# Kernel tuning notes

Measured on AMD Instinct MI355X. Metric: run time of the kernel, lower is better.

## Reference

```python
import jax, jax.numpy as jnp
import numpy as np

H = 1024          # hidden_size
E = 2             # expand factor
D = H * E         # d_inner = 2048
N = 16            # state_size
K = 4             # conv kernel
R = H // 16       # dt_rank = 64
B_SZ = 2
L = 1024
EPS = 1e-6


def setup_inputs() -> dict:
    key = jax.random.key(0)
    ks = jax.random.split(key, 12)
    s = 0.02
    inputs = jax.random.normal(ks[0], (B_SZ, L, H), jnp.float32)
    current_state = jnp.zeros((B_SZ, D, N), jnp.float32)
    norm_w = jnp.ones((H,), jnp.float32)
    in_proj_w = jax.random.normal(ks[1], (2 * D, H), jnp.float32) * s
    in_proj_b = jnp.zeros((2 * D,), jnp.float32)
    conv_w = jax.random.normal(ks[2], (D, 1, K), jnp.float32) * 0.2
    conv_b = jnp.zeros((D,), jnp.float32)
    x_proj_w = jax.random.normal(ks[3], (R + 2 * N, D), jnp.float32) * s
    x_proj_b = jnp.zeros((R + 2 * N,), jnp.float32)
    dt_proj_w = jax.random.normal(ks[4], (D, R), jnp.float32) * s
    dt_proj_b = jnp.zeros((D,), jnp.float32)
    A_log = jnp.log(jnp.tile(jnp.arange(1, N + 1, dtype=jnp.float32)[None, :], (D, 1)))
    D_param = jnp.ones((D,), jnp.float32)
    out_proj_w = jax.random.normal(ks[5], (H, D), jnp.float32) * s
    out_proj_b = jnp.zeros((H,), jnp.float32)
    return dict(inputs=inputs, current_state=current_state, norm_w=norm_w,
                in_proj_w=in_proj_w, in_proj_b=in_proj_b, conv_w=conv_w, conv_b=conv_b,
                x_proj_w=x_proj_w, x_proj_b=x_proj_b, dt_proj_w=dt_proj_w, dt_proj_b=dt_proj_b,
                A_log=A_log, D_param=D_param, out_proj_w=out_proj_w, out_proj_b=out_proj_b)


def _rmsnorm(x, w, eps=EPS):
    var = jnp.mean(x * x, axis=-1, keepdims=True)
    return x * jax.lax.rsqrt(var + eps) * w


def _ssm_forward(inputs, current_state, norm_w, in_proj_w, in_proj_b, conv_w, conv_b,
                 x_proj_w, x_proj_b, dt_proj_w, dt_proj_b, A_log, D_param,
                 out_proj_w, out_proj_b):
    residual = inputs  # standard residual: connect_width -> (inputs, None)
    x = _rmsnorm(inputs, norm_w)                                   # [B,L,H]
    xg = jnp.einsum('blh,oh->blo', x, in_proj_w) + in_proj_b       # [B,L,2D]
    x, gate = jnp.split(xg, 2, axis=-1)                            # each [B,L,D]
    # depthwise causal conv: torch pads K-1 both sides then slices [:L] == left-pad K-1
    xc = jax.lax.conv_general_dilated(
        x.transpose(0, 2, 1), conv_w, window_strides=(1,),
        padding=[(K - 1, 0)], dimension_numbers=('NCH', 'OIH', 'NCH'),
        feature_group_count=D) + conv_b[None, :, None]
    x = jax.nn.silu(xc.transpose(0, 2, 1))                         # [B,L,D]
    proj = jnp.einsum('bld,od->blo', x, x_proj_w) + x_proj_b       # [B,L,R+2N]
    dt, Bm, Cm = proj[..., :R], proj[..., R:R + N], proj[..., R + N:]
    delta = jax.nn.softplus(jnp.einsum('blr,dr->bld', dt, dt_proj_w) + dt_proj_b)  # [B,L,D]
    A = -jnp.exp(A_log)                                            # [D,N]
    log_deltaA = delta[..., None] * A                              # [B,L,D,N] (== log(exp(.)))
    cumsum_deltaA = jnp.exp(jnp.cumsum(log_deltaA, axis=1))        # [B,L,D,N]
    h0_contribution = current_state[:, None] * cumsum_deltaA
    shifted = jnp.concatenate(
        [jnp.ones_like(cumsum_deltaA[:, :1]), cumsum_deltaA[:, :-1]], axis=1)
    deltaB_x = delta[..., None] * Bm[:, :, None, :] * x[..., None] # [B,L,D,N]
    scaled = deltaB_x / jnp.clip(shifted, 1e-10)
    h = jnp.cumsum(scaled, axis=1) * shifted + h0_contribution     # [B,L,D,N]
    y = jnp.sum(h * Cm[:, :, None, :], axis=-1) + x * D_param      # [B,L,D]
    y = y * jax.nn.silu(gate)
    out = jnp.einsum('bld,hd->blh', y, out_proj_w) + out_proj_b    # [B,L,H]
    return residual + out


def reference(inputs, current_state, norm_w, in_proj_w, in_proj_b, conv_w, conv_b,
              x_proj_w, x_proj_b, dt_proj_w, dt_proj_b, A_log, D_param,
              out_proj_w, out_proj_b):
    return _ssm_forward(inputs, current_state, norm_w, in_proj_w, in_proj_b,
                        conv_w, conv_b, x_proj_w, x_proj_b, dt_proj_w, dt_proj_b,
                        A_log, D_param, out_proj_w, out_proj_b)
```

## Files before the change

kernel.cpp:

```cpp
#include <hip/hip_runtime.h>
#include <stdint.h>

#define LSEQ 1024
#define HDIM 1024
#define DDIM 2048
#define BL 2048
#define NST 16
#define XR 1027

typedef unsigned short u16;
typedef __attribute__((ext_vector_type(8))) short bf16x8;
typedef __attribute__((ext_vector_type(4))) float f32x4;

static __device__ __forceinline__ float silu_f(float v) {
  return v * __builtin_amdgcn_rcpf(1.f + __expf(-v));
}
static __device__ __forceinline__ float bf2f(u16 u) {
  union { float f; unsigned int i; } c; c.i = ((unsigned int)u) << 16; return c.f;
}
static __device__ __forceinline__ u16 f2bf(float f) {
  union { float f; unsigned int i; } c; c.f = f;
  unsigned int r = c.i + 0x7fffu + ((c.i >> 16) & 1u);
  return (u16)(r >> 16);
}
static __device__ __forceinline__ float softplus_f(float v) {
  return (v > 20.f) ? v : __logf(1.f + __expf(v));
}

__global__ __launch_bounds__(256) void k_castw(const float* __restrict__ src,
                                               u16* __restrict__ dst) {
  int idx = blockIdx.x * 256 + threadIdx.x;
  float4 v = ((const float4*)src)[idx];
  ushort4 o;
  o.x = f2bf(v.x); o.y = f2bf(v.y); o.z = f2bf(v.z); o.w = f2bf(v.w);
  ((ushort4*)dst)[idx] = o;
}

__global__ __launch_bounds__(256) void k_castsplit(const float* __restrict__ src,
                                                   u16* __restrict__ hi,
                                                   u16* __restrict__ lo) {
  int idx = blockIdx.x * 256 + threadIdx.x;
  float4 v = ((const float4*)src)[idx];
  ushort4 h, l;
  h.x = f2bf(v.x); l.x = f2bf(v.x - bf2f(h.x));
  h.y = f2bf(v.y); l.y = f2bf(v.y - bf2f(h.y));
  h.z = f2bf(v.z); l.z = f2bf(v.z - bf2f(h.z));
  h.w = f2bf(v.w); l.w = f2bf(v.w - bf2f(h.w));
  ((ushort4*)hi)[idx] = h;
  ((ushort4*)lo)[idx] = l;
}

__global__ __launch_bounds__(256) void k_zerohalo(u16* __restrict__ xgb) {
  int idx = blockIdx.x * 256 + threadIdx.x;
  int b = idx / 3072;
  int r = idx - b * 3072;
  ushort4 z4 = {0, 0, 0, 0};
  ((ushort4*)(xgb + (size_t)b * XR * 4096))[r] = z4;
}

__global__ __launch_bounds__(256) void k_rowscale2(const float* __restrict__ inp,
                                                   const float* __restrict__ nw,
                                                   u16* __restrict__ xnb) {
  int row = blockIdx.x;
  int t = threadIdx.x;
  float4 xv = *(const float4*)(inp + (size_t)row * HDIM + t * 4);
  float ss = xv.x * xv.x + xv.y * xv.y + xv.z * xv.z + xv.w * xv.w;
  for (int off = 32; off > 0; off >>= 1) ss += __shfl_down(ss, off);
  __shared__ float red[4];
  if ((t & 63) == 0) red[t >> 6] = ss;
  __syncthreads();
  float tot = red[0] + red[1] + red[2] + red[3];
  float scale = rsqrtf(tot * (1.f / HDIM) + 1e-6f);
  float4 nv = *(const float4*)(nw + t * 4);
  ushort4 o;
  o.x = f2bf(xv.x * scale * nv.x); o.y = f2bf(xv.y * scale * nv.y);
  o.z = f2bf(xv.z * scale * nv.z); o.w = f2bf(xv.w * scale * nv.w);
  ((ushort4*)xnb)[row * 256 + t] = o;
}

__global__ __launch_bounds__(256) void k_gemm1b(const u16* __restrict__ A,
                                                const u16* __restrict__ W,
                                                const float* __restrict__ bias,
                                                u16* __restrict__ xgb) {
  __shared__ u16 Asm[128 * 40];
  __shared__ u16 Wsm[128 * 40];
  int t = threadIdx.x;
  int m0 = blockIdx.y * 128, n0 = blockIdx.x * 128;
  int srow = t >> 1, koff = (t & 1) * 16;
  const u16* Ag = A + (size_t)(m0 + srow) * HDIM + koff;
  const u16* Wg = W + (size_t)(n0 + srow) * HDIM + koff;
  int w = t >> 6, lane = t & 63;
  int wr = w >> 1, wc = w & 1;
  int quad = lane >> 4, mr = lane & 15;
  f32x4 z = {0.f, 0.f, 0.f, 0.f};
  f32x4 acc[4][4] = {{z, z, z, z}, {z, z, z, z}, {z, z, z, z}, {z, z, z, z}};
  const u16* arp = &Asm[(wr * 64 + mr) * 40 + quad * 8];
  const u16* brp = &Wsm[(wc * 64 + mr) * 40 + quad * 8];
  for (int k0 = 0; k0 < HDIM; k0 += 32) {
    uint4 a0 = *(const uint4*)(Ag + k0);
    uint4 a1 = *(const uint4*)(Ag + k0 + 8);
    uint4 w0 = *(const uint4*)(Wg + k0);
    uint4 w1 = *(const uint4*)(Wg + k0 + 8);
    __syncthreads();
    *(uint4*)(&Asm[srow * 40 + koff]) = a0;
    *(uint4*)(&Asm[srow * 40 + koff + 8]) = a1;
    *(uint4*)(&Wsm[srow * 40 + koff]) = w0;
    *(uint4*)(&Wsm[srow * 40 + koff + 8]) = w1;
    __syncthreads();
    bf16x8 af[4], bf[4];
#pragma unroll
    for (int i = 0; i < 4; i++) {
      af[i] = *(const bf16x8*)(arp + i * 16 * 40);
      bf[i] = *(const bf16x8*)(brp + i * 16 * 40);
    }
#pragma unroll
    for (int mi = 0; mi < 4; mi++)
#pragma unroll
      for (int ni = 0; ni < 4; ni++)
        acc[mi][ni] = __builtin_amdgcn_mfma_f32_16x16x32_bf16(af[mi], bf[ni],
                                                              acc[mi][ni], 0, 0, 0);
  }
#pragma unroll
  for (int ni = 0; ni < 4; ni++) {
    int col = n0 + wc * 64 + ni * 16 + mr;
    float bv = bias[col];
#pragma unroll
    for (int mi = 0; mi < 4; mi++) {
#pragma unroll
      for (int rr2 = 0; rr2 < 4; rr2++) {
        int rr = m0 + wr * 64 + mi * 16 + quad * 4 + rr2;
        int row = (rr >> 10) * XR + 3 + (rr & 1023);
        xgb[(size_t)row * 4096 + col] = f2bf(acc[mi][ni][rr2] + bv);
      }
    }
  }
}

__global__ __launch_bounds__(256) void k_gemm2b(const u16* __restrict__ A,
                                                const u16* __restrict__ W,
                                                const float* __restrict__ bias,
                                                const float* __restrict__ resid,
                                                float* __restrict__ out) {
  __shared__ u16 Asm[128 * 40];
  __shared__ u16 Wsm[64 * 40];
  int t = threadIdx.x;
  int m0 = blockIdx.y * 128, n0 = blockIdx.x * 64;
  int srow = t >> 1, koff = (t & 1) * 16;
  const u16* Ag = A + (size_t)(m0 + srow) * DDIM + koff;
  const u16* Wg = W + (size_t)(n0 + (srow & 63)) * DDIM + koff;
  int w = t >> 6, lane = t & 63;
  int wr = w >> 1, wc = w & 1;
  int quad = lane >> 4, mr = lane & 15;
  f32x4 z = {0.f, 0.f, 0.f, 0.f};
  f32x4 acc[4][2] = {{z, z}, {z, z}, {z, z}, {z, z}};
  const u16* arp = &Asm[(wr * 64 + mr) * 40 + quad * 8];
  const u16* brp = &Wsm[(wc * 32 + mr) * 40 + quad * 8];
  for (int k0 = 0; k0 < DDIM; k0 += 32) {
    uint4 a0 = *(const uint4*)(Ag + k0);
    uint4 a1 = *(const uint4*)(Ag + k0 + 8);
    uint4 w0, w1;
    if (t < 128) {
      w0 = *(const uint4*)(Wg + k0);
      w1 = *(const uint4*)(Wg + k0 + 8);
    }
    __syncthreads();
    *(uint4*)(&Asm[srow * 40 + koff]) = a0;
    *(uint4*)(&Asm[srow * 40 + koff + 8]) = a1;
    if (t < 128) {
      *(uint4*)(&Wsm[srow * 40 + koff]) = w0;
      *(uint4*)(&Wsm[srow * 40 + koff + 8]) = w1;
    }
    __syncthreads();
    bf16x8 af[4], bf[2];
#pragma unroll
    for (int i = 0; i < 4; i++) af[i] = *(const bf16x8*)(arp + i * 16 * 40);
#pragma unroll
    for (int i = 0; i < 2; i++) bf[i] = *(const bf16x8*)(brp + i * 16 * 40);
#pragma unroll
    for (int mi = 0; mi < 4; mi++)
#pragma unroll
      for (int ni = 0; ni < 2; ni++)
        acc[mi][ni] = __builtin_amdgcn_mfma_f32_16x16x32_bf16(af[mi], bf[ni],
                                                              acc[mi][ni], 0, 0, 0);
  }
#pragma unroll
  for (int ni = 0; ni < 2; ni++) {
    int col = n0 + wc * 32 + ni * 16 + mr;
    float bv = bias[col];
#pragma unroll
    for (int mi = 0; mi < 4; mi++) {
#pragma unroll
      for (int rr2 = 0; rr2 < 4; rr2++) {
        int row = m0 + wr * 64 + mi * 16 + quad * 4 + rr2;
        out[(size_t)row * HDIM + col] =
            acc[mi][ni][rr2] + bv + resid[(size_t)row * HDIM + col];
      }
    }
  }
}

__global__ __launch_bounds__(256) void k_xprojT(const u16* __restrict__ xgb,
                                                const u16* __restrict__ whb,
                                                const u16* __restrict__ wlb,
                                                const float* __restrict__ cw,
                                                const float* __restrict__ cb,
                                                float* __restrict__ projT,
                                                float* __restrict__ pscr) {
  __shared__ u16 Xst[67 * 40];
  __shared__ u16 XH[64 * 40];
  __shared__ u16 XL[64 * 40];
  __shared__ u16 WH[96 * 40];
  __shared__ u16 WL[96 * 40];
  int t = threadIdx.x;
  int tt = blockIdx.x & 31, ks = blockIdx.x >> 5;
  int tokbase = tt << 6;
  int b = tokbase >> 10, l0 = tokbase & 1023;
  int kbase = ks << 7;
  const u16* xbase = xgb + (size_t)(b * XR + l0) * 4096;
  float* outp = (ks == 0) ? projT : (pscr + (size_t)(ks - 1) * 196608);
  int dlane = t & 31, tokg = t >> 5;
  int wvq = t >> 6, lane = t & 63;
  int quad = lane >> 4, mr = lane & 15;
  f32x4 z = {0.f, 0.f, 0.f, 0.f};
  f32x4 acc[6] = {z, z, z, z, z, z};

  for (int it = 0; it < 4; it++) {
    int kc = kbase + (it << 5);
    for (int idx = t; idx < 268; idx += 256) {
      int r = idx >> 2, p = idx & 3;
      uint4 v = *(const uint4*)(xbase + (size_t)r * 4096 + kc + p * 8);
      *(uint4*)(&Xst[r * 40 + p * 8]) = v;
    }
    for (int idx = t; idx < 384; idx += 256) {
      int r = idx >> 2, p = idx & 3;
      *(uint4*)(&WH[r * 40 + p * 8]) = *(const uint4*)(whb + (size_t)r * 2048 + kc + p * 8);
      *(uint4*)(&WL[r * 40 + p * 8]) = *(const uint4*)(wlb + (size_t)r * 2048 + kc + p * 8);
    }
    __syncthreads();
    {
      int d = kc + dlane;
      float4 cwv = *(const float4*)(cw + d * 4);
      float cbv = cb[d];
      float xr[11];
#pragma unroll
      for (int j = 0; j < 11; j++) xr[j] = bf2f(Xst[(tokg * 8 + j) * 40 + dlane]);
#pragma unroll
      for (int jj = 0; jj < 8; jj++) {
        float xc = silu_f(cbv + cwv.x * xr[jj] + cwv.y * xr[jj + 1] +
                          cwv.z * xr[jj + 2] + cwv.w * xr[jj + 3]);
        u16 h = f2bf(xc);
        u16 l = f2bf(xc - bf2f(h));
        XH[(tokg * 8 + jj) * 40 + dlane] = h;
        XL[(tokg * 8 + jj) * 40 + dlane] = l;
      }
    }
    __syncthreads();
    bf16x8 xh = *(const bf16x8*)(&XH[(wvq * 16 + mr) * 40 + quad * 8]);
    bf16x8 xl = *(const bf16x8*)(&XL[(wvq * 16 + mr) * 40 + quad * 8]);
#pragma unroll
    for (int mi = 0; mi < 6; mi++) {
      bf16x8 wh = *(const bf16x8*)(&WH[(mi * 16 + mr) * 40 + quad * 8]);
      bf16x8 wl = *(const bf16x8*)(&WL[(mi * 16 + mr) * 40 + quad * 8]);
      acc[mi] = __builtin_amdgcn_mfma_f32_16x16x32_bf16(wh, xh, acc[mi], 0, 0, 0);
      acc[mi] = __builtin_amdgcn_mfma_f32_16x16x32_bf16(wh, xl, acc[mi], 0, 0, 0);
      acc[mi] = __builtin_amdgcn_mfma_f32_16x16x32_bf16(wl, xh, acc[mi], 0, 0, 0);
    }
    __syncthreads();
  }
#pragma unroll
  for (int mi = 0; mi < 6; mi++) {
#pragma unroll
    for (int rr = 0; rr < 4; rr++) {
      int o = mi * 16 + quad * 4 + rr;
      outp[(size_t)o * BL + tokbase + wvq * 16 + mr] = acc[mi][rr];
    }
  }
}

__global__ __launch_bounds__(256) void k_xcomb(float* __restrict__ projT,
                                               const float* __restrict__ scr,
                                               const float* __restrict__ xpb) {
  int idx = blockIdx.x * 256 + threadIdx.x;
  int o = idx >> 9;
  float4 a = ((const float4*)projT)[idx];
  float bv = xpb[o];
  float sx = bv, sy = bv, sz = bv, sw = bv;
#pragma unroll
  for (int p = 0; p < 15; p++) {
    float4 s = ((const float4*)(scr + (size_t)p * 196608))[idx];
    sx += s.x; sy += s.y; sz += s.z; sw += s.w;
  }
  a.x += sx; a.y += sy; a.z += sz; a.w += sw;
  ((float4*)projT)[idx] = a;
}

__global__ __launch_bounds__(256) void k_delta(const float* __restrict__ projT,
                                               const float* __restrict__ dtw,
                                               const float* __restrict__ dtb,
                                               float* __restrict__ deltaT) {
  __shared__ float dw_s[16][64];
  int t = threadIdx.x;
  int d0 = (blockIdx.x >> 3) * 16;
  int tokbase = (blockIdx.x & 7) * 256;
  {
    const float* src = dtw + (size_t)d0 * 64;
#pragma unroll
    for (int i = 0; i < 4; i++) {
      int idx = t + i * 256;
      dw_s[idx >> 6][idx & 63] = src[idx];
    }
  }
  __syncthreads();
  int tq = t & 63, dq = t >> 6;
  const float* pr = projT + tokbase + tq * 4;
  int dbase = d0 + dq * 4;
  float acc[4][4];
#pragma unroll
  for (int di = 0; di < 4; di++) {
    float bv = dtb[dbase + di];
    acc[di][0] = bv; acc[di][1] = bv; acc[di][2] = bv; acc[di][3] = bv;
  }
#pragma unroll 8
  for (int r = 0; r < 64; r++) {
    float4 pv = *(const float4*)(pr + (size_t)r * BL);
#pragma unroll
    for (int di = 0; di < 4; di++) {
      float wk = dw_s[dq * 4 + di][r];
      acc[di][0] += pv.x * wk; acc[di][1] += pv.y * wk;
      acc[di][2] += pv.z * wk; acc[di][3] += pv.w * wk;
    }
  }
#pragma unroll
  for (int di = 0; di < 4; di++) {
    float4 o;
    o.x = softplus_f(acc[di][0]); o.y = softplus_f(acc[di][1]);
    o.z = softplus_f(acc[di][2]); o.w = softplus_f(acc[di][3]);
    *(float4*)(deltaT + (size_t)(dbase + di) * BL + tokbase + tq * 4) = o;
  }
}

__global__ __launch_bounds__(256) void k_scan2(const float* __restrict__ projT,
                                               const float* __restrict__ deltaT,
                                               const u16* __restrict__ xgb,
                                               const float* __restrict__ cw,
                                               const float* __restrict__ cb,
                                               const float* __restrict__ alog,
                                               const float* __restrict__ dparam,
                                               const float* __restrict__ cs,
                                               u16* __restrict__ yb) {
  __shared__ float wtot[4];
  __shared__ float xcp[1088];
  __shared__ float uvl[1088];
  __shared__ float dlp[1088];

  int t = threadIdx.x;
  int cidx = ((blockIdx.x & 7) << 9) | (blockIdx.x >> 3);
  int b = cidx >> 11;
  int d = cidx & (DDIM - 1);
  int wv = t >> 6, lane = t & 63;

  float4 cwv = *(const float4*)(cw + d * 4);
  float cbv = cb[d];
  float Dp = dparam[d];
  const u16* xcol = xgb + (size_t)(b * XR + 3) * 4096 + d;
  const u16* gcol = xcol + DDIM;
  u16* ycol = yb + ((size_t)(b << 10)) * DDIM + d;
  int colbase = b << 10;
  int tok0 = t << 2;

  float4 dv = *(const float4*)(deltaT + (size_t)d * BL + colbase + tok0);

  float* xls = dlp;
  if (t < 3) xls[t] = 0.f;
#pragma unroll
  for (int k = 0; k < 4; k++) {
    int tok = t + (k << 8);
    xls[3 + tok] = bf2f(xcol[(size_t)tok * 4096]);
  }
  __syncthreads();

#pragma unroll
  for (int i = 0; i < 4; i++) {
    int tok = tok0 + i;
    float xc = silu_f(cbv + cwv.x * xls[tok] + cwv.y * xls[tok + 1] +
                      cwv.z * xls[tok + 2] + cwv.w * xls[tok + 3]);
    xcp[((tok >> 4) * 17) + (tok & 15)] = xc;
  }
  float d0 = dv.x, d1 = dv.y, d2 = dv.z, d3 = dv.w;
  uvl[((tok0 >> 4) * 17) + (tok0 & 15)]             = d0;
  uvl[(((tok0 + 1) >> 4) * 17) + ((tok0 + 1) & 15)] = d1;
  uvl[(((tok0 + 2) >> 4) * 17) + ((tok0 + 2) & 15)] = d2;
  uvl[(((tok0 + 3) >> 4) * 17) + ((tok0 + 3) & 15)] = d3;
  float c0 = d0, c1 = c0 + d1, c2 = c1 + d2, c3 = c2 + d3;
  float sc = c3;
#pragma unroll
  for (int off = 1; off < 64; off <<= 1) {
    float u = __shfl_up(sc, off);
    if (lane >= off) sc += u;
  }
  if (lane == 63) wtot[wv] = sc;
  __syncthreads();
  {
    float base = sc - c3;
#pragma unroll
    for (int i = 0; i < 3; i++) if (i < wv) base += wtot[i];
    dlp[((tok0 >> 4) * 17) + (tok0 & 15)]             = base + c0;
    dlp[(((tok0 + 1) >> 4) * 17) + ((tok0 + 1) & 15)] = base + c1;
    dlp[(((tok0 + 2) >> 4) * 17) + ((tok0 + 2) & 15)] = base + c2;
    dlp[(((tok0 + 3) >> 4) * 17) + ((tok0 + 3) & 15)] = base + c3;
  }
#pragma unroll
  for (int i = 0; i < 4; i++) {
    int tok = tok0 + i;
    int p = ((tok >> 4) * 17) + (tok & 15);
    uvl[p] = uvl[p] * xcp[p];
  }
  __syncthreads();

  int pb = lane * 17;
  float y[16];
#pragma unroll
  for (int i = 0; i < 16; i++) y[i] = 0.f;
  float Dprev = (lane == 0) ? 0.f : dlp[pb - 2];

#pragma unroll 1
  for (int r = 0; r < 4; r++) {
    int n = (wv << 2) + r;
    float An = -__expf(alog[d * NST + n]);
    float st = cs[(size_t)(b * DDIM + d) * NST + n];
    const float* pB = projT + (size_t)(64 + n) * BL + colbase + (lane << 4);
    const float* pC = pB + (size_t)16 * BL;
    float Pp = __expf(An * Dprev);
    float sl = 0.f;
#pragma unroll
    for (int c = 0; c < 4; c++) {
      float4 bv = *(const float4*)(pB + c * 4);
      float4 cv = *(const float4*)(pC + c * 4);
      float bvs[4] = {bv.x, bv.y, bv.z, bv.w};
      float cvs[4] = {cv.x, cv.y, cv.z, cv.w};
#pragma unroll
      for (int j = 0; j < 4; j++) {
        int i = c * 4 + j;
        float P = __expf(An * dlp[pb + i]);
        float w = uvl[pb + i] * bvs[j] * __builtin_amdgcn_rcpf(fmaxf(Pp, 1e-10f));
        sl += w;
        y[i] += (sl * Pp + st * P) * cvs[j];
        Pp = P;
      }
    }
    float s2 = sl;
#pragma unroll
    for (int off = 1; off < 64; off <<= 1) {
      float u = __shfl_up(s2, off);
      if (lane >= off) s2 += u;
    }
    float Soff = s2 - sl;
#pragma unroll
    for (int c = 0; c < 4; c++) {
      float4 cv = *(const float4*)(pC + c * 4);
      float cvs[4] = {cv.x, cv.y, cv.z, cv.w};
#pragma unroll
      for (int j = 0; j < 4; j++) {
        int i = c * 4 + j;
        float dlm = (i == 0) ? Dprev : dlp[pb + i - 1];
        y[i] += Soff * __expf(An * dlm) * cvs[j];
      }
    }
  }
  __syncthreads();
  if (wv == 2) {
#pragma unroll
    for (int i = 0; i < 16; i++) uvl[pb + i] = y[i];
  } else if (wv == 3) {
#pragma unroll
    for (int i = 0; i < 16; i++) dlp[pb + i] = y[i];
  }
  __syncthreads();
  if (wv == 0) {
#pragma unroll
    for (int i = 0; i < 16; i++) uvl[pb + i] += y[i];
  } else if (wv == 1) {
#pragma unroll
    for (int i = 0; i < 16; i++) dlp[pb + i] += y[i];
  }
  __syncthreads();
#pragma unroll
  for (int i = 0; i < 4; i++) {
    int tok = tok0 + i;
    int p = ((tok >> 4) * 17) + (tok & 15);
    float yv = uvl[p] + dlp[p] + xcp[p] * Dp;
    float g = bf2f(gcol[(size_t)tok * 4096]);
    ycol[(size_t)tok * DDIM] = f2bf(yv * silu_f(g));
  }
}

extern "C" void kernel_launch(void* const* d_in, const int* in_sizes, int n_in,
                              void* d_out, int out_size, void* d_ws, size_t ws_size,
                              hipStream_t stream) {
  const float* inp    = (const float*)d_in[0];
  const float* cstate = (const float*)d_in[1];
  const float* norm_w = (const float*)d_in[2];
  const float* w1     = (const float*)d_in[3];
  const float* b1     = (const float*)d_in[4];
  const float* convw  = (const float*)d_in[5];
  const float* convb  = (const float*)d_in[6];
  const float* xpw    = (const float*)d_in[7];
  const float* xpb    = (const float*)d_in[8];
  const float* dtw    = (const float*)d_in[9];
  const float* dtb    = (const float*)d_in[10];
  const float* alog   = (const float*)d_in[11];
  const float* dparam = (const float*)d_in[12];
  const float* wo     = (const float*)d_in[13];
  const float* bo     = (const float*)d_in[14];
  float* out = (float*)d_out;

  char* wsb = (char*)d_ws;
  u16*   w1b    = (u16*)(wsb + 0);
  u16*   wob    = (u16*)(wsb + 8388608);
  u16*   whb    = (u16*)(wsb + 12591104);
  u16*   wlb    = (u16*)(wsb + 12984320);
  float* projT  = (float*)(wsb + 13377536);
  u16*   xgb    = (u16*)(wsb + 14163968);
  u16*   yb     = (u16*)(wsb + 30990336);
  u16*   xnb    = yb;
  float* deltaT = (float*)(wsb + 39378944);
  float* pscr   = deltaT;

  k_castw<<<4096, 256, 0, stream>>>(w1, w1b);
  k_castw<<<2048, 256, 0, stream>>>(wo, wob);
  k_castsplit<<<192, 256, 0, stream>>>(xpw, whb, wlb);
  k_rowscale2<<<BL, 256, 0, stream>>>(inp, norm_w, xnb);
  k_gemm1b<<<dim3(32, 16), 256, 0, stream>>>(xnb, w1b, b1, xgb);
  k_zerohalo<<<24, 256, 0, stream>>>(xgb);
  k_xprojT<<<512, 256, 0, stream>>>(xgb, whb, wlb, convw, convb, projT, pscr);
  k_xcomb<<<192, 256, 0, stream>>>(projT, pscr, xpb);
  k_delta<<<1024, 256, 0, stream>>>(projT, dtw, dtb, deltaT);
  k_scan2<<<2 * DDIM, 256, 0, stream>>>(projT, deltaT, xgb, convw, convb,
                                        alog, dparam, cstate, yb);
  k_gemm2b<<<dim3(16, 16), 256, 0, stream>>>(yb, wob, bo, inp, out);
}
```

Baseline: 290.6 us.

## Fuse prep kernels, pre-transpose x for scan, split-K the out projection

Merges the three weight-cast kernels and the halo zeroing into one launch. Adds a tiled transpose kernel so the scan reads the x column contiguously instead of with a 4096-element stride. Splits the output projection GEMM into two K halves so twice as many blocks run, then sums the partials with bias and residual in a separate combine kernel. This trades extra launches and partial-sum traffic for better occupancy and coalescing, and reuses the w1b and deltaT workspace regions once they are no longer needed.

```diff
diff --git a/kernel.cpp b/kernel.cpp
--- a/kernel.cpp
+++ b/kernel.cpp
@@ -27,35 +27,45 @@
   return (v > 20.f) ? v : __logf(1.f + __expf(v));
 }
 
-__global__ __launch_bounds__(256) void k_castw(const float* __restrict__ src,
-                                               u16* __restrict__ dst) {
-  int idx = blockIdx.x * 256 + threadIdx.x;
-  float4 v = ((const float4*)src)[idx];
-  ushort4 o;
-  o.x = f2bf(v.x); o.y = f2bf(v.y); o.z = f2bf(v.z); o.w = f2bf(v.w);
-  ((ushort4*)dst)[idx] = o;
-}
-
-__global__ __launch_bounds__(256) void k_castsplit(const float* __restrict__ src,
-                                                   u16* __restrict__ hi,
-                                                   u16* __restrict__ lo) {
-  int idx = blockIdx.x * 256 + threadIdx.x;
-  float4 v = ((const float4*)src)[idx];
-  ushort4 h, l;
-  h.x = f2bf(v.x); l.x = f2bf(v.x - bf2f(h.x));
-  h.y = f2bf(v.y); l.y = f2bf(v.y - bf2f(h.y));
-  h.z = f2bf(v.z); l.z = f2bf(v.z - bf2f(h.z));
-  h.w = f2bf(v.w); l.w = f2bf(v.w - bf2f(h.w));
-  ((ushort4*)hi)[idx] = h;
-  ((ushort4*)lo)[idx] = l;
-}
-
-__global__ __launch_bounds__(256) void k_zerohalo(u16* __restrict__ xgb) {
-  int idx = blockIdx.x * 256 + threadIdx.x;
-  int b = idx / 3072;
-  int r = idx - b * 3072;
-  ushort4 z4 = {0, 0, 0, 0};
-  ((ushort4*)(xgb + (size_t)b * XR * 4096))[r] = z4;
+__global__ __launch_bounds__(256) void k_prep(const float* __restrict__ w1,
+                                              u16* __restrict__ w1b,
+                                              const float* __restrict__ wo,
+                                              u16* __restrict__ wob,
+                                              const float* __restrict__ xpw,
+                                              u16* __restrict__ whb,
+                                              u16* __restrict__ wlb,
+                                              u16* __restrict__ xgb) {
+  int bidx = blockIdx.x;
+  int t = threadIdx.x;
+  if (bidx < 4096) {
+    int idx = bidx * 256 + t;
+    float4 v = ((const float4*)w1)[idx];
+    ushort4 o;
+    o.x = f2bf(v.x); o.y = f2bf(v.y); o.z = f2bf(v.z); o.w = f2bf(v.w);
+    ((ushort4*)w1b)[idx] = o;
+  } else if (bidx < 6144) {
+    int idx = (bidx - 4096) * 256 + t;
+    float4 v = ((const float4*)wo)[idx];
+    ushort4 o;
+    o.x = f2bf(v.x); o.y = f2bf(v.y); o.z = f2bf(v.z); o.w = f2bf(v.w);
+    ((ushort4*)wob)[idx] = o;
+  } else if (bidx < 6336) {
+    int idx = (bidx - 6144) * 256 + t;
+    float4 v = ((const float4*)xpw)[idx];
+    ushort4 h, l;
+    h.x = f2bf(v.x); l.x = f2bf(v.x - bf2f(h.x));
+    h.y = f2bf(v.y); l.y = f2bf(v.y - bf2f(h.y));
+    h.z = f2bf(v.z); l.z = f2bf(v.z - bf2f(h.z));
+    h.w = f2bf(v.w); l.w = f2bf(v.w - bf2f(h.w));
+    ((ushort4*)whb)[idx] = h;
+    ((ushort4*)wlb)[idx] = l;
+  } else {
+    int idx = (bidx - 6336) * 256 + t;
+    int b = idx / 3072;
+    int r = idx - b * 3072;
+    ushort4 z4 = {0, 0, 0, 0};
+    ((ushort4*)(xgb + (size_t)b * XR * 4096))[r] = z4;
+  }
 }
 
 __global__ __launch_bounds__(256) void k_rowscale2(const float* __restrict__ inp,
@@ -136,18 +146,47 @@
   }
 }
 
+__global__ __launch_bounds__(256) void k_xT(const u16* __restrict__ xgb,
+                                            u16* __restrict__ xT) {
+  __shared__ u16 tile[64][66];
+  int dt = blockIdx.x & 31;
+  int tt = blockIdx.x >> 5;
+  int gtok0 = tt << 6;
+  int b = gtok0 >> 10, l0 = gtok0 & 1023;
+  int d0 = dt << 6;
+  int t = threadIdx.x;
+  const u16* src = xgb + (size_t)(b * XR + 3 + l0) * 4096 + d0;
+#pragma unroll
+  for (int i = 0; i < 8; i++) {
+    int idx = t + i * 256;
+    int row = idx >> 5, uc = idx & 31;
+    unsigned int v = *(const unsigned int*)(src + (size_t)row * 4096 + uc * 2);
+    tile[row][uc * 2]     = (u16)(v & 0xffffu);
+    tile[row][uc * 2 + 1] = (u16)(v >> 16);
+  }
+  __syncthreads();
+#pragma unroll
+  for (int i = 0; i < 8; i++) {
+    int idx = t + i * 256;
+    int r = idx >> 5, c2 = idx & 31;
+    unsigned int lo = tile[c2 * 2][r];
+    unsigned int hi = tile[c2 * 2 + 1][r];
+    *(unsigned int*)(xT + (size_t)(d0 + r) * 2048 + gtok0 + c2 * 2) = lo | (hi << 16);
+  }
+}
+
 __global__ __launch_bounds__(256) void k_gemm2b(const u16* __restrict__ A,
                                                 const u16* __restrict__ W,
-                                                const float* __restrict__ bias,
-                                                const float* __restrict__ resid,
-                                                float* __restrict__ out) {
+                                                float* __restrict__ psplit) {
   __shared__ u16 Asm[128 * 40];
   __shared__ u16 Wsm[64 * 40];
   int t = threadIdx.x;
   int m0 = blockIdx.y * 128, n0 = blockIdx.x * 64;
+  int kstart = blockIdx.z << 10;
+  float* outp = psplit + (size_t)blockIdx.z * 2048 * 1024;
   int srow = t >> 1, koff = (t & 1) * 16;
-  const u16* Ag = A + (size_t)(m0 + srow) * DDIM + koff;
-  const u16* Wg = W + (size_t)(n0 + (srow & 63)) * DDIM + koff;
+  const u16* Ag = A + (size_t)(m0 + srow) * DDIM + kstart + koff;
+  const u16* Wg = W + (size_t)(n0 + (srow & 63)) * DDIM + kstart + koff;
   int w = t >> 6, lane = t & 63;
   int wr = w >> 1, wc = w & 1;
   int quad = lane >> 4, mr = lane & 15;
@@ -155,7 +194,7 @@
   f32x4 acc[4][2] = {{z, z}, {z, z}, {z, z}, {z, z}};
   const u16* arp = &Asm[(wr * 64 + mr) * 40 + quad * 8];
   const u16* brp = &Wsm[(wc * 32 + mr) * 40 + quad * 8];
-  for (int k0 = 0; k0 < DDIM; k0 += 32) {
+  for (int k0 = 0; k0 < 1024; k0 += 32) {
     uint4 a0 = *(const uint4*)(Ag + k0);
     uint4 a1 = *(const uint4*)(Ag + k0 + 8);
     uint4 w0, w1;
@@ -186,17 +225,33 @@
 #pragma unroll
   for (int ni = 0; ni < 2; ni++) {
     int col = n0 + wc * 32 + ni * 16 + mr;
-    float bv = bias[col];
 #pragma unroll
     for (int mi = 0; mi < 4; mi++) {
 #pragma unroll
       for (int rr2 = 0; rr2 < 4; rr2++) {
         int row = m0 + wr * 64 + mi * 16 + quad * 4 + rr2;
-        out[(size_t)row * HDIM + col] =
-            acc[mi][ni][rr2] + bv + resid[(size_t)row * HDIM + col];
+        outp[(size_t)row * 1024 + col] = acc[mi][ni][rr2];
       }
     }
   }
+}
+
+__global__ __launch_bounds__(256) void k_ocomb(const float* __restrict__ psplit,
+                                               const float* __restrict__ bias,
+                                               const float* __restrict__ resid,
+                                               float* __restrict__ out) {
+  int idx = blockIdx.x * 256 + threadIdx.x;
+  int colf = idx & 255;
+  float4 a = ((const float4*)psplit)[idx];
+  float4 b2 = ((const float4*)(psplit + 2048 * 1024))[idx];
+  float4 rv = ((const float4*)resid)[idx];
+  float4 bv = *(const float4*)(bias + colf * 4);
+  float4 o;
+  o.x = a.x + b2.x + bv.x + rv.x;
+  o.y = a.y + b2.y + bv.y + rv.y;
+  o.z = a.z + b2.z + bv.z + rv.z;
+  o.w = a.w + b2.w + bv.w + rv.w;
+  ((float4*)out)[idx] = o;
 }
 
 __global__ __launch_bounds__(256) void k_xprojT(const u16* __restrict__ xgb,
@@ -341,6 +396,7 @@
 
 __global__ __launch_bounds__(256) void k_scan2(const float* __restrict__ projT,
                                                const float* __restrict__ deltaT,
+                                               const u16* __restrict__ xT,
                                                const u16* __restrict__ xgb,
                                                const float* __restrict__ cw,
                                                const float* __restrict__ cb,
@@ -362,8 +418,7 @@
   float4 cwv = *(const float4*)(cw + d * 4);
   float cbv = cb[d];
   float Dp = dparam[d];
-  const u16* xcol = xgb + (size_t)(b * XR + 3) * 4096 + d;
-  const u16* gcol = xcol + DDIM;
+  const u16* gcol = xgb + (size_t)(b * XR + 3) * 4096 + d + DDIM;
   u16* ycol = yb + ((size_t)(b << 10)) * DDIM + d;
   int colbase = b << 10;
   int tok0 = t << 2;
@@ -372,10 +427,12 @@
 
   float* xls = dlp;
   if (t < 3) xls[t] = 0.f;
-#pragma unroll
-  for (int k = 0; k < 4; k++) {
-    int tok = t + (k << 8);
-    xls[3 + tok] = bf2f(xcol[(size_t)tok * 4096]);
+  {
+    ushort4 xv = ((const ushort4*)(xT + (size_t)d * 2048 + colbase))[t];
+    xls[3 + tok0 + 0] = bf2f(xv.x);
+    xls[3 + tok0 + 1] = bf2f(xv.y);
+    xls[3 + tok0 + 2] = bf2f(xv.z);
+    xls[3 + tok0 + 3] = bf2f(xv.w);
   }
   __syncthreads();
 
@@ -516,6 +573,7 @@
 
   char* wsb = (char*)d_ws;
   u16*   w1b    = (u16*)(wsb + 0);
+  u16*   xTbuf  = w1b;
   u16*   wob    = (u16*)(wsb + 8388608);
   u16*   whb    = (u16*)(wsb + 12591104);
   u16*   wlb    = (u16*)(wsb + 12984320);
@@ -525,17 +583,17 @@
   u16*   xnb    = yb;
   float* deltaT = (float*)(wsb + 39378944);
   float* pscr   = deltaT;
-
-  k_castw<<<4096, 256, 0, stream>>>(w1, w1b);
-  k_castw<<<2048, 256, 0, stream>>>(wo, wob);
-  k_castsplit<<<192, 256, 0, stream>>>(xpw, whb, wlb);
+  float* psplit = deltaT;
+
+  k_prep<<<6360, 256, 0, stream>>>(w1, w1b, wo, wob, xpw, whb, wlb, xgb);
   k_rowscale2<<<BL, 256, 0, stream>>>(inp, norm_w, xnb);
   k_gemm1b<<<dim3(32, 16), 256, 0, stream>>>(xnb, w1b, b1, xgb);
-  k_zerohalo<<<24, 256, 0, stream>>>(xgb);
+  k_xT<<<1024, 256, 0, stream>>>(xgb, xTbuf);
   k_xprojT<<<512, 256, 0, stream>>>(xgb, whb, wlb, convw, convb, projT, pscr);
   k_xcomb<<<192, 256, 0, stream>>>(projT, pscr, xpb);
   k_delta<<<1024, 256, 0, stream>>>(projT, dtw, dtb, deltaT);
-  k_scan2<<<2 * DDIM, 256, 0, stream>>>(projT, deltaT, xgb, convw, convb,
+  k_scan2<<<2 * DDIM, 256, 0, stream>>>(projT, deltaT, xTbuf, xgb, convw, convb,
                                         alog, dparam, cstate, yb);
-  k_gemm2b<<<dim3(16, 16), 256, 0, stream>>>(yb, wob, bo, inp, out);
-}
+  k_gemm2b<<<dim3(16, 16, 2), 256, 0, stream>>>(yb, wob, psplit);
+  k_ocomb<<<2048, 256, 0, stream>>>(psplit, bo, inp, out);
+}
```

New measurement: 274.2 us. 5.6% less time.
